# Optimization experiments

Measured on AMD Instinct MI355X. Metric: run time of the kernel, lower is better.

## Reference

```python
import jax, jax.numpy as jnp
import numpy as np

B, S, D, H = 4, 2048, 768, 12
HD = D // H

def rope_cos_sin(seq_len, head_dim, dtype=jnp.float32):
    inv_freq = 1.0 / (10000.0 ** (jnp.arange(0, head_dim, 2, dtype=jnp.float32) / head_dim))
    ang = jnp.arange(seq_len, dtype=jnp.float32)[:, None] * inv_freq[None, :]  # (S, HD/2)
    cos = jnp.concatenate([jnp.cos(ang), jnp.cos(ang)], axis=-1).astype(dtype)  # (S, HD)
    sin = jnp.concatenate([jnp.sin(ang), jnp.sin(ang)], axis=-1).astype(dtype)
    return cos, sin

def rotate_half(x):
    x1, x2 = jnp.split(x, 2, axis=-1)
    return jnp.concatenate([-x2, x1], axis=-1)

def setup_inputs() -> dict:
    key = jax.random.key(0)
    k0, k1, k2, k3, k4 = jax.random.split(key, 5)
    s = 0.02
    return {
        "embeds": jax.random.normal(k0, (B, S, D), jnp.float32),
        "Wq": jax.random.normal(k1, (D, D), jnp.float32) * s,
        "Wk": jax.random.normal(k2, (D, D), jnp.float32) * s,
        "Wv": jax.random.normal(k3, (D, D), jnp.float32) * s,
        "Wo": jax.random.normal(k4, (D, D), jnp.float32) * s,
        "bo": jnp.zeros((D,), jnp.float32),
    }

def reference(embeds, Wq, Wk, Wv, Wo, bo):
    b, n, d = embeds.shape
    scale = 1.0 / np.sqrt(HD)
    # projections (torch Linear: x @ W.T), reshape to (b, H, n, HD)
    def proj(W):
        return (embeds @ W.T).reshape(b, n, H, HD).transpose(0, 2, 1, 3)
    q, k, v = proj(Wq), proj(Wk), proj(Wv)
    cos, sin = rope_cos_sin(n, HD)  # (n, HD)
    cos, sin = cos[None, None], sin[None, None]
    q = q * cos + rotate_half(q) * sin
    k = k * cos + rotate_half(k) * sin
    scores = jnp.einsum('bhqd,bhkd->bhqk', q, k)
    causal = jnp.triu(jnp.ones((n, n), bool), k=1)
    scores = jnp.where(causal, -jnp.inf, scores) * scale
    attn = jax.nn.softmax(scores, axis=-1)
    ctx = jnp.einsum('bhqk,bhkd->bhqd', attn, v)
    ctx = ctx.transpose(0, 2, 1, 3).reshape(b, n, d)
    return ctx @ Wo.T + bo
```

## Files before the change

### kernel.cpp

```cpp
#include <hip/hip_runtime.h>

using bf16x8 = __attribute__((ext_vector_type(8))) short;
using f32x4  = __attribute__((ext_vector_type(4))) float;

#define DEVI __device__ __forceinline__

static constexpr int S_LEN = 2048, D_MODEL = 768, NH = 12, HDIM = 64;
static constexpr float QSCALE = 0.125f * 1.4426950408889634f;

DEVI unsigned short f2bf(float x) {
    unsigned u = __builtin_bit_cast(unsigned, x);
    u += 0x7fffu + ((u >> 16) & 1u);
    return (unsigned short)(u >> 16);
}

#define GLL16(gsrc, ldst) __builtin_amdgcn_global_load_lds( \
    (const __attribute__((address_space(1))) void*)(gsrc),  \
    (__attribute__((address_space(3))) void*)(ldst), 16, 0, 0)

DEVI bf16x8 lds_frag(const unsigned short* lds, int row, int cb) {
    return *(const bf16x8*)((const char*)lds + row * 128 + (cb ^ ((row & 7) << 4)));
}

__global__ void cvt_kernel(const float* __restrict__ src, unsigned short* __restrict__ dst, int n4) {
    int i = blockIdx.x * blockDim.x + threadIdx.x;
    if (i >= n4) return;
    float4 v = reinterpret_cast<const float4*>(src)[i];
    ushort4 o;
    o.x = f2bf(v.x); o.y = f2bf(v.y); o.z = f2bf(v.z); o.w = f2bf(v.w);
    reinterpret_cast<ushort4*>(dst)[i] = o;
}

__global__ void rope_kernel(float* __restrict__ cos_t, float* __restrict__ sin_t) {
    int idx = blockIdx.x * 64 + threadIdx.x;
    int s = idx >> 5, f = idx & 31;
    float inv = exp2f(-(float)f * (13.287712379549449f / 32.0f));
    float ang = (float)s * inv;
    cos_t[idx] = cosf(ang);
    sin_t[idx] = sinf(ang);
}

DEVI void stage128x64(const unsigned short* __restrict__ g, unsigned short* lds,
                      int ldg, int row0, int k0, int wave, int lane) {
    int rl = lane >> 3;
    int cb = (lane & 7) << 4;
    #pragma unroll
    for (int i = 0; i < 4; ++i) {
        int r = wave * 32 + i * 8 + rl;
        const char* src = (const char*)(g + (size_t)(row0 + r) * ldg + k0) + (cb ^ ((r & 7) << 4));
        GLL16(src, lds + (wave * 32 + i * 8) * 64);
    }
}

DEVI void gemm_core(const unsigned short* __restrict__ Ag, const unsigned short* __restrict__ Bg,
                    int m0, int n0, int K, int lda, int ldb,
                    unsigned short* As, unsigned short* Bs, f32x4 acc[4][4]) {
    int tid = threadIdx.x, wave = tid >> 6, lane = tid & 63;
    int wr = wave >> 1, wc = wave & 1, lrow = lane & 15, lk = lane >> 4;
    #pragma unroll
    for (int mi = 0; mi < 4; ++mi)
        #pragma unroll
        for (int ni = 0; ni < 4; ++ni) acc[mi][ni] = f32x4{0.f, 0.f, 0.f, 0.f};
    for (int k0 = 0; k0 < K; k0 += 64) {
        stage128x64(Ag, As, lda, m0, k0, wave, lane);
        stage128x64(Bg, Bs, ldb, n0, k0, wave, lane);
        __syncthreads();
        #pragma unroll
        for (int kk = 0; kk < 2; ++kk) {
            bf16x8 a[4], b[4];
            #pragma unroll
            for (int mi = 0; mi < 4; ++mi) a[mi] = lds_frag(As, wr * 64 + mi * 16 + lrow, kk * 64 + lk * 16);
            #pragma unroll
            for (int ni = 0; ni < 4; ++ni) b[ni] = lds_frag(Bs, wc * 64 + ni * 16 + lrow, kk * 64 + lk * 16);
            __builtin_amdgcn_s_setprio(1);
            #pragma unroll
            for (int mi = 0; mi < 4; ++mi)
                #pragma unroll
                for (int ni = 0; ni < 4; ++ni)
                    acc[mi][ni] = __builtin_amdgcn_mfma_f32_16x16x32_bf16(a[mi], b[ni], acc[mi][ni], 0, 0, 0);
            __builtin_amdgcn_s_setprio(0);
        }
        __syncthreads();
    }
}

__global__ __launch_bounds__(256) void qkv_kernel(
        const unsigned short* __restrict__ Xg,
        const unsigned short* __restrict__ Wqg, const unsigned short* __restrict__ Wkg,
        const unsigned short* __restrict__ Wvg,
        const float* __restrict__ cos_t, const float* __restrict__ sin_t,
        unsigned short* __restrict__ Qo, unsigned short* __restrict__ Ko,
        unsigned short* __restrict__ Vt) {
    __shared__ unsigned short sbuf[128 * 128];
    unsigned short* As = sbuf;
    unsigned short* Bs = sbuf + 128 * 64;
    int z = blockIdx.z;
    const unsigned short* Wg = (z == 0) ? Wqg : ((z == 1) ? Wkg : Wvg);
    int m0 = blockIdx.x * 128, n0 = blockIdx.y * 128;
    f32x4 acc[4][4];
    gemm_core(Xg, Wg, m0, n0, D_MODEL, D_MODEL, D_MODEL, As, Bs, acc);

    int tid = threadIdx.x, wave = tid >> 6, lane = tid & 63;
    int wr = wave >> 1, wc = wave & 1, lrow = lane & 15, lk = lane >> 4;

    if (z < 2) {
        unsigned short* O = (z == 0) ? Qo : Ko;
        float qs = (z == 0) ? QSCALE : 1.0f;
        int h = blockIdx.y * 2 + wc;
        #pragma unroll
        for (int mi = 0; mi < 4; ++mi) {
            #pragma unroll
            for (int r = 0; r < 4; ++r) {
                int m = m0 + wr * 64 + mi * 16 + lk * 4 + r;
                int bb = m >> 11, spos = m & 2047;
                size_t base = ((size_t)(bb * NH + h) * S_LEN + spos) * HDIM;
                #pragma unroll
                for (int nf = 0; nf < 2; ++nf) {
                    int hd = nf * 16 + lrow;
                    float c = cos_t[spos * 32 + hd], sn = sin_t[spos * 32 + hd];
                    float x1 = acc[mi][nf][r], x2 = acc[mi][nf + 2][r];
                    O[base + hd]      = f2bf((x1 * c - x2 * sn) * qs);
                    O[base + hd + 32] = f2bf((x2 * c + x1 * sn) * qs);
                }
            }
        }
    } else {
        unsigned short* T = sbuf;
        #pragma unroll
        for (int mi = 0; mi < 4; ++mi)
            #pragma unroll
            for (int nt = 0; nt < 4; ++nt) {
                int hd  = wc * 64 + nt * 16 + lrow;
                int sp0 = wr * 64 + mi * 16 + lk * 4;
                ushort4 pk;
                pk.x = f2bf(acc[mi][nt][0]); pk.y = f2bf(acc[mi][nt][1]);
                pk.z = f2bf(acc[mi][nt][2]); pk.w = f2bf(acc[mi][nt][3]);
                *(ushort4*)((char*)T + ((hd * 256 + sp0 * 2) ^ ((hd & 7) << 4))) = pk;
            }
        __syncthreads();
        int hd = tid >> 1, half = tid & 1;
        int h  = blockIdx.y * 2 + (hd >> 6), hdh = hd & 63;
        int bb = m0 >> 11, sp_abs = (m0 & 2047) + half * 64;
        unsigned short* dst = Vt + ((size_t)(bb * NH + h) * HDIM + hdh) * S_LEN + sp_abs;
        #pragma unroll
        for (int j = 0; j < 8; ++j) {
            bf16x8 v = *(const bf16x8*)((const char*)T +
                        ((hd * 256 + half * 128 + j * 16) ^ ((hd & 7) << 4)));
            *(bf16x8*)((char*)dst + j * 16) = v;
        }
    }
}

DEVI void attn_stage(const unsigned short* __restrict__ Kb, const unsigned short* __restrict__ Vt,
                     unsigned short* Ksb, unsigned short* Vsb,
                     int bh, int kv0, int wave, int lane) {
    int rl = lane >> 3, cb = (lane & 7) << 4;
    #pragma unroll
    for (int i = 0; i < 2; ++i) {
        int r = wave * 16 + i * 8 + rl;
        int scb = cb ^ ((r & 7) << 4);
        const char* srck = (const char*)(Kb + ((size_t)bh * S_LEN + kv0 + r) * HDIM) + scb;
        GLL16(srck, Ksb + (wave * 16 + i * 8) * 64);
        const char* srcv = (const char*)(Vt + ((size_t)bh * HDIM + r) * S_LEN + kv0) + scb;
        GLL16(srcv, Vsb + (wave * 16 + i * 8) * 64);
    }
}

DEVI void do_qkt_sw(const bf16x8 (&kf)[2][4], bf16x8 qf0, bf16x8 qf1, f32x4 (&sc)[4]) {
    #pragma unroll
    for (int nt = 0; nt < 4; ++nt) sc[nt] = f32x4{0.f, 0.f, 0.f, 0.f};
    __builtin_amdgcn_s_setprio(1);
    #pragma unroll
    for (int kk = 0; kk < 2; ++kk) {
        bf16x8 qf = kk ? qf1 : qf0;
        #pragma unroll
        for (int nt = 0; nt < 4; ++nt)
            sc[nt] = __builtin_amdgcn_mfma_f32_16x16x32_bf16(kf[kk][nt], qf, sc[nt], 0, 0, 0);
    }
    __builtin_amdgcn_s_setprio(0);
}

template <bool DIAG>
DEVI void do_softmax_sw(const f32x4 (&sc)[4], unsigned short* Pw, f32x4 o[4],
                        float& mrow, float& lsum, int lrow, int lk, int qrel) {
    float t[16];
    float mx = -__builtin_inff();
    #pragma unroll
    for (int nt = 0; nt < 4; ++nt)
        #pragma unroll
        for (int r = 0; r < 4; ++r) {
            float v = sc[nt][r];
            if (DIAG && (nt * 16 + lk * 4 + r > qrel)) v = -__builtin_inff();
            t[nt * 4 + r] = v;
            mx = fmaxf(mx, v);
        }
    mx = fmaxf(mx, __shfl_xor(mx, 16, 64));
    mx = fmaxf(mx, __shfl_xor(mx, 32, 64));
    float mnew = fmaxf(mrow, mx);
    float alpha = exp2f(mrow - mnew);
    mrow = mnew;
    float ps = 0.f;
    #pragma unroll
    for (int nt = 0; nt < 4; ++nt) {
        ushort4 pk;
        float p0 = exp2f(t[nt * 4 + 0] - mnew), p1 = exp2f(t[nt * 4 + 1] - mnew);
        float p2 = exp2f(t[nt * 4 + 2] - mnew), p3 = exp2f(t[nt * 4 + 3] - mnew);
        ps += (p0 + p1) + (p2 + p3);
        pk.x = f2bf(p0); pk.y = f2bf(p1); pk.z = f2bf(p2); pk.w = f2bf(p3);
        *(ushort4*)((char*)Pw + lrow * 128 + (((nt * 16 + lk * 4) * 2) ^ ((lrow & 7) << 4))) = pk;
    }
    ps += __shfl_xor(ps, 16, 64);
    ps += __shfl_xor(ps, 32, 64);
    lsum = lsum * alpha + ps;
    #pragma unroll
    for (int nt = 0; nt < 4; ++nt) o[nt] *= alpha;
}

DEVI void do_pv_sw(const unsigned short* Vs, const unsigned short* Pw, f32x4 o[4],
                   int lrow, int lk) {
    __builtin_amdgcn_s_setprio(1);
    #pragma unroll
    for (int kk = 0; kk < 2; ++kk) {
        bf16x8 pf = lds_frag(Pw, lrow, kk * 64 + lk * 16);
        #pragma unroll
        for (int nt = 0; nt < 4; ++nt) {
            bf16x8 vf = lds_frag(Vs, nt * 16 + lrow, kk * 64 + lk * 16);
            o[nt] = __builtin_amdgcn_mfma_f32_16x16x32_bf16(vf, pf, o[nt], 0, 0, 0);
        }
    }
    __builtin_amdgcn_s_setprio(0);
}

DEVI void attn_epilogue(const f32x4 o[4], float lsum, int qt, int bh,
                        unsigned short* __restrict__ Ctx, int lrow, int lk, int wave) {
    float inv = 1.0f / lsum;
    int b = bh / NH, h = bh % NH;
    int spos = qt * 64 + wave * 16 + lrow;
    size_t base = ((size_t)(b * S_LEN + spos)) * D_MODEL + h * HDIM;
    #pragma unroll
    for (int nt = 0; nt < 4; ++nt) {
        ushort4 pk;
        pk.x = f2bf(o[nt][0] * inv); pk.y = f2bf(o[nt][1] * inv);
        pk.z = f2bf(o[nt][2] * inv); pk.w = f2bf(o[nt][3] * inv);
        *(ushort4*)(Ctx + base + nt * 16 + lk * 4) = pk;
    }
}

__global__ __launch_bounds__(256, 3) void attn_kernel(
        const unsigned short* __restrict__ Q, const unsigned short* __restrict__ Kb,
        const unsigned short* __restrict__ Vt, unsigned short* __restrict__ Ctx) {
    __shared__ unsigned short Ks[2][64 * 64], Vs[2][64 * 64], Ps[4][2][16 * 64];
    int id = blockIdx.x;
    int n  = (id & 7) * 96 + (id >> 3);
    int bh = n >> 4;
    int pj = n & 15;
    int qa = pj, qb = 31 - pj;
    int tid = threadIdx.x, wave = tid >> 6, lane = tid & 63;
    int lrow = lane & 15, lk = lane >> 4;
    int qrel = wave * 16 + lrow;

    const unsigned short* qpa = Q + ((size_t)bh * S_LEN + qa * 64 + qrel) * HDIM;
    const unsigned short* qpb = Q + ((size_t)bh * S_LEN + qb * 64 + qrel) * HDIM;
    bf16x8 qfa0 = *(const bf16x8*)(qpa + lk * 8);
    bf16x8 qfa1 = *(const bf16x8*)(qpa + 32 + lk * 8);
    bf16x8 qfb0 = *(const bf16x8*)(qpb + lk * 8);
    bf16x8 qfb1 = *(const bf16x8*)(qpb + 32 + lk * 8);

    f32x4 oa[4], ob[4];
    float ma = -__builtin_inff(), la = 0.f, mb = -__builtin_inff(), lb = 0.f;
    #pragma unroll
    for (int nt = 0; nt < 4; ++nt) { oa[nt] = f32x4{0.f, 0.f, 0.f, 0.f}; ob[nt] = f32x4{0.f, 0.f, 0.f, 0.f}; }

    attn_stage(Kb, Vt, Ks[0], Vs[0], bh, 0, wave, lane);
    int cur = 0;
    f32x4 sc[4];
    for (int kt = 0; kt <= qb; ++kt) {
        __syncthreads();
        if (kt < qb) attn_stage(Kb, Vt, Ks[cur ^ 1], Vs[cur ^ 1], bh, (kt + 1) * 64, wave, lane);

        bf16x8 kf[2][4];
        #pragma unroll
        for (int kk = 0; kk < 2; ++kk)
            #pragma unroll
            for (int nt = 0; nt < 4; ++nt)
                kf[kk][nt] = lds_frag(Ks[cur], nt * 16 + lrow, kk * 64 + lk * 16);

        if (kt <= qa) {
            do_qkt_sw(kf, qfa0, qfa1, sc);
            if (kt == qa) do_softmax_sw<true >(sc, Ps[wave][0], oa, ma, la, lrow, lk, qrel);
            else          do_softmax_sw<false>(sc, Ps[wave][0], oa, ma, la, lrow, lk, qrel);
            do_pv_sw(Vs[cur], Ps[wave][0], oa, lrow, lk);
        }
        do_qkt_sw(kf, qfb0, qfb1, sc);
        if (kt == qb) do_softmax_sw<true >(sc, Ps[wave][1], ob, mb, lb, lrow, lk, qrel);
        else          do_softmax_sw<false>(sc, Ps[wave][1], ob, mb, lb, lrow, lk, qrel);
        do_pv_sw(Vs[cur], Ps[wave][1], ob, lrow, lk);
        cur ^= 1;
    }

    attn_epilogue(oa, la, qa, bh, Ctx, lrow, lk, wave);
    attn_epilogue(ob, lb, qb, bh, Ctx, lrow, lk, wave);
}

__global__ __launch_bounds__(256) void outproj_kernel(
        const unsigned short* __restrict__ Cg, const unsigned short* __restrict__ Wog,
        const float* __restrict__ bo, float* __restrict__ Out) {
    __shared__ unsigned short As[128 * 64], Bs[128 * 64];
    int m0 = blockIdx.x * 128, n0 = blockIdx.y * 128;
    f32x4 acc[4][4];
    gemm_core(Cg, Wog, m0, n0, D_MODEL, D_MODEL, D_MODEL, As, Bs, acc);

    int tid = threadIdx.x, wave = tid >> 6, lane = tid & 63;
    int wr = wave >> 1, wc = wave & 1, lrow = lane & 15, lk = lane >> 4;
    #pragma unroll
    for (int mi = 0; mi < 4; ++mi)
        #pragma unroll
        for (int r = 0; r < 4; ++r) {
            int m = m0 + wr * 64 + mi * 16 + lk * 4 + r;
            #pragma unroll
            for (int nt = 0; nt < 4; ++nt) {
                int n = n0 + wc * 64 + nt * 16 + lrow;
                Out[(size_t)m * D_MODEL + n] = acc[mi][nt][r] + bo[n];
            }
        }
}

extern "C" void kernel_launch(void* const* d_in, const int* in_sizes, int n_in,
                              void* d_out, int out_size, void* d_ws, size_t ws_size,
                              hipStream_t stream) {
    const float* embeds = (const float*)d_in[0];
    const float* Wq = (const float*)d_in[1];
    const float* Wk = (const float*)d_in[2];
    const float* Wv = (const float*)d_in[3];
    const float* Wo = (const float*)d_in[4];
    const float* bo = (const float*)d_in[5];
    float* out = (float*)d_out;

    const size_t NE = (size_t)4 * 2048 * 768;
    const size_t NW = (size_t)768 * 768;

    unsigned short* ws     = (unsigned short*)d_ws;
    unsigned short* emb_bf = ws;
    unsigned short* wq_bf  = emb_bf + NE;
    unsigned short* wk_bf  = wq_bf + NW;
    unsigned short* wv_bf  = wk_bf + NW;
    unsigned short* wo_bf  = wv_bf + NW;
    unsigned short* qb     = wo_bf + NW;
    unsigned short* kb     = qb + NE;
    unsigned short* vt     = kb + NE;
    float* cos_t = (float*)(vt + NE);
    float* sin_t = cos_t + 2048 * 32;
    unsigned short* ctx = emb_bf;

    cvt_kernel<<<dim3((unsigned)((NE / 4 + 255) / 256)), 256, 0, stream>>>(embeds, emb_bf, (int)(NE / 4));
    cvt_kernel<<<dim3((unsigned)((NW / 4 + 255) / 256)), 256, 0, stream>>>(Wq, wq_bf, (int)(NW / 4));
    cvt_kernel<<<dim3((unsigned)((NW / 4 + 255) / 256)), 256, 0, stream>>>(Wk, wk_bf, (int)(NW / 4));
    cvt_kernel<<<dim3((unsigned)((NW / 4 + 255) / 256)), 256, 0, stream>>>(Wv, wv_bf, (int)(NW / 4));
    cvt_kernel<<<dim3((unsigned)((NW / 4 + 255) / 256)), 256, 0, stream>>>(Wo, wo_bf, (int)(NW / 4));
    rope_kernel<<<dim3(1024), 64, 0, stream>>>(cos_t, sin_t);

    qkv_kernel<<<dim3(64, 6, 3), 256, 0, stream>>>(emb_bf, wq_bf, wk_bf, wv_bf,
                                                   cos_t, sin_t, qb, kb, vt);
    attn_kernel<<<dim3(768), 256, 0, stream>>>(qb, kb, vt, ctx);
    outproj_kernel<<<dim3(64, 6), 256, 0, stream>>>(ctx, wo_bf, bo, out);
}
```

Measured before the change: 164.6 us.

## Use packed bf16 converts, lazy softmax rescale, interleaved QK^T, and higher occupancy

Replaces the software f32-to-bf16 rounding with the hardware v_cvt_pk_bf16_f32 instruction in the V-transpose, softmax and epilogue stores. Adds a lazy online-softmax rescale that skips the alpha multiply unless some row max grows by more than 8 in log2 units, and uses a tree-shaped max reduction. Both QK^T products for the paired query tiles are issued before their softmax and PV steps so their MFMAs can overlap. The P scratch buffer is shared between the two tiles and launch bounds rise to 4 blocks per CU, which adds register pressure and a possible LDS hazard: tile A's PV reads of the shared P buffer must finish before tile B's softmax writes it, with no barrier between them.

New measurement: 197.2 us. 1.2x slower.

```diff
diff --git a/kernel.cpp b/kernel.cpp
--- a/kernel.cpp
+++ b/kernel.cpp
@@ -12,6 +12,12 @@
     unsigned u = __builtin_bit_cast(unsigned, x);
     u += 0x7fffu + ((u >> 16) & 1u);
     return (unsigned short)(u >> 16);
+}
+
+DEVI unsigned cvt_pk_bf16(float lo, float hi) {
+    unsigned r;
+    asm("v_cvt_pk_bf16_f32 %0, %1, %2" : "=v"(r) : "v"(lo), "v"(hi));
+    return r;
 }
 
 #define GLL16(gsrc, ldst) __builtin_amdgcn_global_load_lds( \
@@ -132,10 +138,10 @@
             for (int nt = 0; nt < 4; ++nt) {
                 int hd  = wc * 64 + nt * 16 + lrow;
                 int sp0 = wr * 64 + mi * 16 + lk * 4;
-                ushort4 pk;
-                pk.x = f2bf(acc[mi][nt][0]); pk.y = f2bf(acc[mi][nt][1]);
-                pk.z = f2bf(acc[mi][nt][2]); pk.w = f2bf(acc[mi][nt][3]);
-                *(ushort4*)((char*)T + ((hd * 256 + sp0 * 2) ^ ((hd & 7) << 4))) = pk;
+                uint2 pk;
+                pk.x = cvt_pk_bf16(acc[mi][nt][0], acc[mi][nt][1]);
+                pk.y = cvt_pk_bf16(acc[mi][nt][2], acc[mi][nt][3]);
+                *(uint2*)((char*)T + ((hd * 256 + sp0 * 2) ^ ((hd & 7) << 4))) = pk;
             }
         __syncthreads();
         int hd = tid >> 1, half = tid & 1;
@@ -184,7 +190,6 @@
 DEVI void do_softmax_sw(const f32x4 (&sc)[4], unsigned short* Pw, f32x4 o[4],
                         float& mrow, float& lsum, int lrow, int lk, int qrel) {
     float t[16];
-    float mx = -__builtin_inff();
     #pragma unroll
     for (int nt = 0; nt < 4; ++nt)
         #pragma unroll
@@ -192,28 +197,36 @@
             float v = sc[nt][r];
             if (DIAG && (nt * 16 + lk * 4 + r > qrel)) v = -__builtin_inff();
             t[nt * 4 + r] = v;
-            mx = fmaxf(mx, v);
-        }
+        }
+    float m0 = fmaxf(fmaxf(t[0], t[1]),  fmaxf(t[2], t[3]));
+    float m1 = fmaxf(fmaxf(t[4], t[5]),  fmaxf(t[6], t[7]));
+    float m2 = fmaxf(fmaxf(t[8], t[9]),  fmaxf(t[10], t[11]));
+    float m3 = fmaxf(fmaxf(t[12], t[13]), fmaxf(t[14], t[15]));
+    float mx = fmaxf(fmaxf(m0, m1), fmaxf(m2, m3));
     mx = fmaxf(mx, __shfl_xor(mx, 16, 64));
     mx = fmaxf(mx, __shfl_xor(mx, 32, 64));
-    float mnew = fmaxf(mrow, mx);
-    float alpha = exp2f(mrow - mnew);
-    mrow = mnew;
+    if (!__all(mx <= mrow + 8.0f)) {
+        float mnew = fmaxf(mrow, mx);
+        float alpha = exp2f(mrow - mnew);
+        mrow = mnew;
+        lsum *= alpha;
+        #pragma unroll
+        for (int nt = 0; nt < 4; ++nt) o[nt] *= alpha;
+    }
     float ps = 0.f;
     #pragma unroll
     for (int nt = 0; nt < 4; ++nt) {
-        ushort4 pk;
-        float p0 = exp2f(t[nt * 4 + 0] - mnew), p1 = exp2f(t[nt * 4 + 1] - mnew);
-        float p2 = exp2f(t[nt * 4 + 2] - mnew), p3 = exp2f(t[nt * 4 + 3] - mnew);
+        float p0 = exp2f(t[nt * 4 + 0] - mrow), p1 = exp2f(t[nt * 4 + 1] - mrow);
+        float p2 = exp2f(t[nt * 4 + 2] - mrow), p3 = exp2f(t[nt * 4 + 3] - mrow);
         ps += (p0 + p1) + (p2 + p3);
-        pk.x = f2bf(p0); pk.y = f2bf(p1); pk.z = f2bf(p2); pk.w = f2bf(p3);
-        *(ushort4*)((char*)Pw + lrow * 128 + (((nt * 16 + lk * 4) * 2) ^ ((lrow & 7) << 4))) = pk;
+        uint2 pk;
+        pk.x = cvt_pk_bf16(p0, p1);
+        pk.y = cvt_pk_bf16(p2, p3);
+        *(uint2*)((char*)Pw + lrow * 128 + (((nt * 16 + lk * 4) * 2) ^ ((lrow & 7) << 4))) = pk;
     }
     ps += __shfl_xor(ps, 16, 64);
     ps += __shfl_xor(ps, 32, 64);
-    lsum = lsum * alpha + ps;
-    #pragma unroll
-    for (int nt = 0; nt < 4; ++nt) o[nt] *= alpha;
+    lsum += ps;
 }
 
 DEVI void do_pv_sw(const unsigned short* Vs, const unsigned short* Pw, f32x4 o[4],
@@ -239,17 +252,17 @@
     size_t base = ((size_t)(b * S_LEN + spos)) * D_MODEL + h * HDIM;
     #pragma unroll
     for (int nt = 0; nt < 4; ++nt) {
-        ushort4 pk;
-        pk.x = f2bf(o[nt][0] * inv); pk.y = f2bf(o[nt][1] * inv);
-        pk.z = f2bf(o[nt][2] * inv); pk.w = f2bf(o[nt][3] * inv);
-        *(ushort4*)(Ctx + base + nt * 16 + lk * 4) = pk;
-    }
-}
-
-__global__ __launch_bounds__(256, 3) void attn_kernel(
+        uint2 pk;
+        pk.x = cvt_pk_bf16(o[nt][0] * inv, o[nt][1] * inv);
+        pk.y = cvt_pk_bf16(o[nt][2] * inv, o[nt][3] * inv);
+        *(uint2*)(Ctx + base + nt * 16 + lk * 4) = pk;
+    }
+}
+
+__global__ __launch_bounds__(256, 4) void attn_kernel(
         const unsigned short* __restrict__ Q, const unsigned short* __restrict__ Kb,
         const unsigned short* __restrict__ Vt, unsigned short* __restrict__ Ctx) {
-    __shared__ unsigned short Ks[2][64 * 64], Vs[2][64 * 64], Ps[4][2][16 * 64];
+    __shared__ unsigned short Ks[2][64 * 64], Vs[2][64 * 64], Ps[4][16 * 64];
     int id = blockIdx.x;
     int n  = (id & 7) * 96 + (id >> 3);
     int bh = n >> 4;
@@ -273,7 +286,7 @@
 
     attn_stage(Kb, Vt, Ks[0], Vs[0], bh, 0, wave, lane);
     int cur = 0;
-    f32x4 sc[4];
+    f32x4 sca[4], scb[4];
     for (int kt = 0; kt <= qb; ++kt) {
         __syncthreads();
         if (kt < qb) attn_stage(Kb, Vt, Ks[cur ^ 1], Vs[cur ^ 1], bh, (kt + 1) * 64, wave, lane);
@@ -285,16 +298,18 @@
             for (int nt = 0; nt < 4; ++nt)
                 kf[kk][nt] = lds_frag(Ks[cur], nt * 16 + lrow, kk * 64 + lk * 16);
 
-        if (kt <= qa) {
-            do_qkt_sw(kf, qfa0, qfa1, sc);
-            if (kt == qa) do_softmax_sw<true >(sc, Ps[wave][0], oa, ma, la, lrow, lk, qrel);
-            else          do_softmax_sw<false>(sc, Ps[wave][0], oa, ma, la, lrow, lk, qrel);
-            do_pv_sw(Vs[cur], Ps[wave][0], oa, lrow, lk);
-        }
-        do_qkt_sw(kf, qfb0, qfb1, sc);
-        if (kt == qb) do_softmax_sw<true >(sc, Ps[wave][1], ob, mb, lb, lrow, lk, qrel);
-        else          do_softmax_sw<false>(sc, Ps[wave][1], ob, mb, lb, lrow, lk, qrel);
-        do_pv_sw(Vs[cur], Ps[wave][1], ob, lrow, lk);
+        bool doA = (kt <= qa);
+        if (doA) do_qkt_sw(kf, qfa0, qfa1, sca);
+        do_qkt_sw(kf, qfb0, qfb1, scb);
+
+        if (doA) {
+            if (kt == qa) do_softmax_sw<true >(sca, Ps[wave], oa, ma, la, lrow, lk, qrel);
+            else          do_softmax_sw<false>(sca, Ps[wave], oa, ma, la, lrow, lk, qrel);
+            do_pv_sw(Vs[cur], Ps[wave], oa, lrow, lk);
+        }
+        if (kt == qb) do_softmax_sw<true >(scb, Ps[wave], ob, mb, lb, lrow, lk, qrel);
+        else          do_softmax_sw<false>(scb, Ps[wave], ob, mb, lb, lrow, lk, qrel);
+        do_pv_sw(Vs[cur], Ps[wave], ob, lrow, lk);
         cur ^= 1;
     }
 
```
